# Kernel optimization log

Measured on AMD Instinct MI355X. Metric: run time of the kernel, lower is better.

The kernel has to match this reference:

```python
import jax, jax.numpy as jnp
import numpy as np

N, E, H, NOISE, T, G = 50000, 400000, 128, 64, 128, 16
EPS = 1e-5


def _graph_norm(x, seg, num_seg, w, b, ms):
    # PyG GraphNorm: per-graph mean/std with learnable mean_scale
    cnt = jnp.maximum(jax.ops.segment_sum(jnp.ones((x.shape[0],), x.dtype), seg, num_segments=num_seg), 1.0)
    mean = jax.ops.segment_sum(x, seg, num_segments=num_seg) / cnt[:, None]
    out = x - mean[seg] * ms
    var = jax.ops.segment_sum(out * out, seg, num_segments=num_seg) / cnt[:, None]
    return w * out / jnp.sqrt(var + EPS)[seg] + b


def _forward(features, noise_mapping_emb, time_emb,
             We, be, Wp, bp, Wq, bq, Wr, br, Wu, bu, Wv, bv,
             gnh_w, gnh_b, gnh_ms, gne_w, gne_b, gne_ms,
             Wt, bt, ln_w, ln_b, Wo, bo,
             edge_mapping_idx, batch):
    src, dst = edge_mapping_idx[0], edge_mapping_idx[1]
    nme = noise_mapping_emb @ We + be                                  # [E,H]
    e_hat = nme @ Wp + bp + (features @ Wq + bq)[src] + (features @ Wr + br)[dst]
    gates = jax.nn.sigmoid(e_hat)
    aggr = jax.ops.segment_sum((features @ Wv + bv)[dst] * gates, src, num_segments=N)
    h = _graph_norm(features @ Wu + bu + aggr, batch, G, gnh_w, gnh_b, gnh_ms)
    eseg = batch[src]                                                  # edge -> graph
    e = _graph_norm(e_hat, eseg, G, gne_w, gne_b, gne_ms)
    h = jax.nn.relu(h)
    e = jax.nn.relu(e)
    e = e + (jax.nn.relu(time_emb) @ Wt + bt)[eseg]
    h = features + h
    # out_layer: LayerNorm -> SiLU -> Linear
    mu = jnp.mean(e, axis=-1, keepdims=True)
    var = jnp.mean((e - mu) ** 2, axis=-1, keepdims=True)
    ln = (e - mu) / jnp.sqrt(var + EPS) * ln_w + ln_b
    e = nme + jax.nn.silu(ln) @ Wo + bo
    return h, e


def setup_inputs() -> dict:
    key = jax.random.key(0)
    ks = jax.random.split(key, 16)

    def lin(k, i, o):
        k1, k2 = jax.random.split(k)
        s = 1.0 / np.sqrt(i)
        return (jax.random.uniform(k1, (i, o), minval=-s, maxval=s, dtype=jnp.float32),
                jax.random.uniform(k2, (o,), minval=-s, maxval=s, dtype=jnp.float32))

    We, be = lin(ks[5], NOISE, H)
    Wp, bp = lin(ks[6], H, H)
    Wq, bq = lin(ks[7], H, H)
    Wr, br = lin(ks[8], H, H)
    Wu, bu = lin(ks[9], H, H)
    Wv, bv = lin(ks[10], H, H)
    Wt, bt = lin(ks[11], T, H)
    Wo, bo = lin(ks[12], H, H)
    ones = jnp.ones((H,), jnp.float32)
    zeros = jnp.zeros((H,), jnp.float32)
    return dict(
        features=jax.random.normal(ks[0], (N, H), dtype=jnp.float32),
        edge_mapping_idx=jax.random.randint(ks[1], (2, E), 0, N),
        noise_mapping_emb=jax.random.normal(ks[2], (E, NOISE), dtype=jnp.float32),
        time_emb=jax.random.normal(ks[3], (G, T), dtype=jnp.float32),
        batch=jnp.sort(jax.random.randint(ks[4], (N,), 0, G)),
        We=We, be=be, Wp=Wp, bp=bp, Wq=Wq, bq=bq, Wr=Wr, br=br,
        Wu=Wu, bu=bu, Wv=Wv, bv=bv,
        gnh_w=ones, gnh_b=zeros, gnh_ms=ones,
        gne_w=ones, gne_b=zeros, gne_ms=ones,
        Wt=Wt, bt=bt, ln_w=ones, ln_b=zeros, Wo=Wo, bo=bo,
    )


def reference(features, edge_mapping_idx, noise_mapping_emb, time_emb, batch,
              We, be, Wp, bp, Wq, bq, Wr, br, Wu, bu, Wv, bv,
              gnh_w, gnh_b, gnh_ms, gne_w, gne_b, gne_ms,
              Wt, bt, ln_w, ln_b, Wo, bo):
    return _forward(features, noise_mapping_emb, time_emb,
                    We, be, Wp, bp, Wq, bq, Wr, br, Wu, bu, Wv, bv,
                    gnh_w, gnh_b, gnh_ms, gne_w, gne_b, gne_ms,
                    Wt, bt, ln_w, ln_b, Wo, bo,
                    edge_mapping_idx, batch)
```

## Files before the change

kernel.cpp:

```cpp
#include <hip/hip_runtime.h>

#define NN 50000
#define NE 400000
#define HD 128
#define ND 64
#define GG 16
#define EPSV 1e-5f
#define ETILE 64
#define ETILE2 128

#define SLEN (2 * GG * HD + GG)
#define PSTRIDE 4352
#define EP 512
#define HP 256

typedef unsigned short u16;
typedef unsigned int   u32;
typedef unsigned char  u8;
typedef __attribute__((__ext_vector_type__(8))) __bf16 bf16x8;
typedef __attribute__((__ext_vector_type__(4))) float  f32x4;

__device__ __forceinline__ float us2f(u16 u) { return __uint_as_float(((u32)u) << 16); }
__device__ __forceinline__ u16 f2us(float f) {
    u32 u = __float_as_uint(f);
    u += 0x7fffu + ((u >> 16) & 1u);
    return (u16)(u >> 16);
}
__device__ __forceinline__ float sigmoidf_(float x) { return 1.f / (1.f + __expf(-x)); }

__global__ __launch_bounds__(256) void wep_kernel(
    const float* __restrict__ We, const float* __restrict__ Wp,
    const float* __restrict__ be, const float* __restrict__ bp,
    float* __restrict__ Wep, float* __restrict__ bep)
{
    __shared__ float wp[HD][HD];
    const int t = threadIdx.x;
    for (int i = t; i < HD * HD; i += 256) wp[i >> 7][i & 127] = Wp[i];
    __syncthreads();
    const int c = t & 127;
    for (int r = blockIdx.x * 4 + (t >> 7); r < (blockIdx.x + 1) * 4 && r < ND; r += 2) {
        float a = 0.f;
        for (int k = 0; k < HD; ++k) a = fmaf(We[r * HD + k], wp[k][c], a);
        Wep[r * HD + c] = a;
    }
    if (blockIdx.x == 0 && t < HD) {
        float a = bp[t];
        for (int k = 0; k < HD; ++k) a = fmaf(be[k], wp[k][t], a);
        bep[t] = a;
    }
}

__global__ __launch_bounds__(256) void prep_all_kernel(
    const float* __restrict__ Wq, const float* __restrict__ Wr,
    const float* __restrict__ Wv, const float* __restrict__ Wu,
    const float* __restrict__ Wo, const float* __restrict__ Wep,
    const float* __restrict__ We,
    u16* __restrict__ WqT, u16* __restrict__ WrT, u16* __restrict__ WvT,
    u16* __restrict__ WuT, u16* __restrict__ WoT, u16* __restrict__ WepT,
    u16* __restrict__ WeT)
{
    const float* in; u16* out; int K;
    switch (blockIdx.y) {
        case 0: in = Wq;  out = WqT;  K = HD; break;
        case 1: in = Wr;  out = WrT;  K = HD; break;
        case 2: in = Wv;  out = WvT;  K = HD; break;
        case 3: in = Wu;  out = WuT;  K = HD; break;
        case 4: in = Wo;  out = WoT;  K = HD; break;
        case 5: in = Wep; out = WepT; K = ND; break;
        default: in = We; out = WeT;  K = ND; break;
    }
    int idx = blockIdx.x * 256 + threadIdx.x;
    if (idx >= K * HD) return;
    int k = idx >> 7, n = idx & 127;
    out[n * K + k] = f2us(in[idx]);
}

__global__ __launch_bounds__(256) void hist_kernel(
    const int* __restrict__ srcArr, u32* __restrict__ deg)
{
    int e = blockIdx.x * 256 + threadIdx.x;
    if (e >= NE) return;
    atomicAdd(&deg[srcArr[e]], 1u);
}

#define SCAN_C 49
__global__ __launch_bounds__(1024) void scan_kernel(
    const u32* __restrict__ deg, int* __restrict__ start)
{
    __shared__ u32 sums[1024];
    const int t = threadIdx.x;
    const int i0 = t * SCAN_C;
    u32 tot = 0;
    for (int j = 0; j < SCAN_C; ++j) { int i = i0 + j; if (i < NN) tot += deg[i]; }
    sums[t] = tot;
    __syncthreads();
    for (int off = 1; off < 1024; off <<= 1) {
        u32 v = (t >= off) ? sums[t - off] : 0u;
        __syncthreads();
        sums[t] += v;
        __syncthreads();
    }
    u32 run = (t == 0) ? 0u : sums[t - 1];
    for (int j = 0; j < SCAN_C; ++j) {
        int i = i0 + j;
        if (i < NN) { start[i] = (int)run; run += deg[i]; }
    }
    if (t == 1023) start[NN] = (int)run;
}

__global__ __launch_bounds__(256) void scatter_kernel(
    const int* __restrict__ srcArr, const int* __restrict__ dstArr,
    const int* __restrict__ batch, const int* __restrict__ start,
    u32* __restrict__ cnt2, int* __restrict__ perm,
    int* __restrict__ src_csr, int* __restrict__ dst_csr,
    u8* __restrict__ g8csr)
{
    int e = blockIdx.x * 256 + threadIdx.x;
    if (e >= NE) return;
    int s = srcArr[e];
    u32 pos = atomicAdd(&cnt2[s], 1u);
    int j = start[s] + (int)pos;
    perm[j] = e;
    src_csr[j] = s;
    dst_csr[j] = dstArr[e];
    g8csr[j] = (u8)batch[s];
}

__global__ __launch_bounds__(256) void proj4_kernel(
    const float* __restrict__ feat,
    const u16* __restrict__ WqT, const u16* __restrict__ WrT,
    const u16* __restrict__ WvT, const u16* __restrict__ WuT,
    const float* __restrict__ bq, const float* __restrict__ br,
    const float* __restrict__ bv, const float* __restrict__ bu,
    u16* __restrict__ fq, u16* __restrict__ fr, u16* __restrict__ fv,
    float* __restrict__ fu32)
{
    __shared__ __align__(16) u16 As[ETILE * HD];
    const int t = threadIdx.x;
    const int rbase = blockIdx.x * ETILE;
    #pragma unroll
    for (int i = 0; i < 16; ++i) {
        int idx2 = t + i * 256;
        int row = idx2 >> 6, p = idx2 & 63;
        int grow = rbase + row;
        float2 v = make_float2(0.f, 0.f);
        if (grow < NN) v = *reinterpret_cast<const float2*>(&feat[(size_t)grow * HD + p * 2]);
        u32 pk = (u32)f2us(v.x) | ((u32)f2us(v.y) << 16);
        int off = (row * 256 + p * 4) ^ ((row & 7) << 4);
        *reinterpret_cast<u32*>(reinterpret_cast<char*>(As) + off) = pk;
    }
    __syncthreads();
    const int w = t >> 6, lane = t & 63;
    const int rt = w * 16, l15 = lane & 15, kg = lane >> 4;
    const int lrow = rt + l15;
    bf16x8 afr[4];
    #pragma unroll
    for (int kk = 0; kk < 4; ++kk) {
        int off = (lrow * 256 + (kk * 32 + kg * 8) * 2) ^ ((lrow & 7) << 4);
        afr[kk] = *reinterpret_cast<const bf16x8*>(reinterpret_cast<const char*>(As) + off);
    }
    const u16* WTs[4] = {WqT, WrT, WvT, WuT};
    const float* Bs2[4] = {bq, br, bv, bu};
    u16* Os[3] = {fq, fr, fv};
    #pragma unroll
    for (int m = 0; m < 4; ++m) {
        f32x4 acc[8];
        #pragma unroll
        for (int nt = 0; nt < 8; ++nt) { acc[nt][0]=0.f; acc[nt][1]=0.f; acc[nt][2]=0.f; acc[nt][3]=0.f; }
        const u16* W = WTs[m];
        #pragma unroll
        for (int nt = 0; nt < 8; ++nt) {
            #pragma unroll
            for (int kk = 0; kk < 4; ++kk) {
                bf16x8 b = *reinterpret_cast<const bf16x8*>(&W[(nt * 16 + l15) * HD + kk * 32 + kg * 8]);
                acc[nt] = __builtin_amdgcn_mfma_f32_16x16x32_bf16(afr[kk], b, acc[nt], 0, 0, 0);
            }
        }
        #pragma unroll
        for (int nt = 0; nt < 8; ++nt) {
            int gcol = nt * 16 + l15;
            float bias = Bs2[m][gcol];
            #pragma unroll
            for (int i = 0; i < 4; ++i) {
                int grow = rbase + rt + kg * 4 + i;
                if (grow < NN) {
                    float v = acc[nt][i] + bias;
                    if (m < 3) Os[m][(size_t)grow * HD + gcol] = f2us(v);
                    else       fu32[(size_t)grow * HD + gcol] = v;
                }
            }
        }
    }
}

__global__ __launch_bounds__(256) void ehat_kernel(
    const float* __restrict__ noise, const u16* __restrict__ WepT,
    const float* __restrict__ bep,
    const u16* __restrict__ fq, const u16* __restrict__ fr,
    const int* __restrict__ perm, const int* __restrict__ src_csr,
    const int* __restrict__ dst_csr,
    u16* __restrict__ ehat_csr)
{
    const int t = threadIdx.x;
    const int rbase = blockIdx.x * ETILE;
    const int w = t >> 6, lane = t & 63;
    const int rt = w * 16, l15 = lane & 15, kg = lane >> 4;
    const int jl = rbase + rt + l15;
    const int el = perm[jl];
    u32 an[2][4];
    #pragma unroll
    for (int kk = 0; kk < 2; ++kk) {
        const int c = kk * 32 + kg * 8;
        float4 n0 = *reinterpret_cast<const float4*>(&noise[(size_t)el * ND + c]);
        float4 n1 = *reinterpret_cast<const float4*>(&noise[(size_t)el * ND + c + 4]);
        an[kk][0] = (u32)f2us(n0.x) | ((u32)f2us(n0.y) << 16);
        an[kk][1] = (u32)f2us(n0.z) | ((u32)f2us(n0.w) << 16);
        an[kk][2] = (u32)f2us(n1.x) | ((u32)f2us(n1.y) << 16);
        an[kk][3] = (u32)f2us(n1.z) | ((u32)f2us(n1.w) << 16);
    }
    f32x4 acc[8];
    #pragma unroll
    for (int nt = 0; nt < 8; ++nt) {
        float b = bep[nt * 16 + l15];
        acc[nt][0] = b; acc[nt][1] = b; acc[nt][2] = b; acc[nt][3] = b;
    }
    #pragma unroll
    for (int nt = 0; nt < 8; ++nt) {
        #pragma unroll
        for (int kk = 0; kk < 2; ++kk) {
            bf16x8 b = *reinterpret_cast<const bf16x8*>(&WepT[(nt * 16 + l15) * ND + kk * 32 + kg * 8]);
            acc[nt] = __builtin_amdgcn_mfma_f32_16x16x32_bf16(
                *reinterpret_cast<const bf16x8*>(an[kk]), b, acc[nt], 0, 0, 0);
        }
    }
    #pragma unroll
    for (int i = 0; i < 4; ++i) {
        int jrow = rbase + rt + kg * 4 + i;
        int s = src_csr[jrow], d = dst_csr[jrow];
        #pragma unroll
        for (int nt = 0; nt < 8; ++nt) {
            int gcol = nt * 16 + l15;
            float v = acc[nt][i]
                    + us2f(fq[(size_t)s * HD + gcol]) + us2f(fr[(size_t)d * HD + gcol]);
            ehat_csr[(size_t)jrow * HD + gcol] = f2us(v);
        }
    }
}

__global__ __launch_bounds__(256) void aggr_kernel(
    const u16* __restrict__ ehat_csr, const u16* __restrict__ fv,
    const int* __restrict__ dst_csr, const int* __restrict__ start,
    float* __restrict__ xout)
{
    const int w = threadIdx.x >> 6, lane = threadIdx.x & 63;
    const int c0 = lane * 2;
    for (int node = blockIdx.x * 4 + w; node < NN; node += gridDim.x * 4) {
        int s0 = start[node], s1 = start[node + 1];
        float2 uv = *reinterpret_cast<const float2*>(&xout[(size_t)node * HD + c0]);
        float a0 = 0.f, a1 = 0.f;
        for (int j = s0; j < s1; ++j) {
            int d = dst_csr[j];
            u32 ev = *reinterpret_cast<const u32*>(&ehat_csr[(size_t)j * HD + c0]);
            u32 vv = *reinterpret_cast<const u32*>(&fv[(size_t)d * HD + c0]);
            a0 = fmaf(sigmoidf_(us2f((u16)ev)),         us2f((u16)vv),         a0);
            a1 = fmaf(sigmoidf_(us2f((u16)(ev >> 16))), us2f((u16)(vv >> 16)), a1);
        }
        *reinterpret_cast<float2*>(&xout[(size_t)node * HD + c0]) =
            make_float2(a0 + uv.x, a1 + uv.y);
    }
}

__global__ __launch_bounds__(256) void hstats_part_kernel(
    const float* __restrict__ xout, const int* __restrict__ batch,
    float* __restrict__ hpart)
{
    __shared__ float sm[SLEN];
    const int t = threadIdx.x;
    for (int i = t; i < SLEN; i += 256) sm[i] = 0.f;
    __syncthreads();
    const int cg = t & 15, rq = t >> 4;
    const int c8 = cg * 8;
    const int chunk = (NN + HP - 1) / HP;
    const int rstart = blockIdx.x * chunk;
    const int rend = min(NN, rstart + chunk);
    float s0[8], z0[8];
    #pragma unroll
    for (int p = 0; p < 8; ++p) { s0[p] = 0.f; z0[p] = 0.f; }
    float cn = 0.f;
    int curg = -1;
    for (int row = rstart + rq; row < rend; row += 16) {
        int g = batch[row];
        if (g != curg) {
            if (curg >= 0) {
                #pragma unroll
                for (int p = 0; p < 8; ++p) {
                    unsafeAtomicAdd(&sm[curg * HD + c8 + p], s0[p]);
                    unsafeAtomicAdd(&sm[2048 + curg * HD + c8 + p], z0[p]);
                    s0[p] = 0.f; z0[p] = 0.f;
                }
                if (cg == 0) { unsafeAtomicAdd(&sm[4096 + curg], cn); }
                cn = 0.f;
            }
            curg = g;
        }
        float4 xa = *reinterpret_cast<const float4*>(&xout[(size_t)row * HD + c8]);
        float4 xb = *reinterpret_cast<const float4*>(&xout[(size_t)row * HD + c8 + 4]);
        const float xs8[8] = {xa.x, xa.y, xa.z, xa.w, xb.x, xb.y, xb.z, xb.w};
        #pragma unroll
        for (int p = 0; p < 8; ++p) { s0[p] += xs8[p]; z0[p] = fmaf(xs8[p], xs8[p], z0[p]); }
        cn += (cg == 0) ? 1.f : 0.f;
    }
    if (curg >= 0) {
        #pragma unroll
        for (int p = 0; p < 8; ++p) {
            unsafeAtomicAdd(&sm[curg * HD + c8 + p], s0[p]);
            unsafeAtomicAdd(&sm[2048 + curg * HD + c8 + p], z0[p]);
        }
        if (cg == 0) { unsafeAtomicAdd(&sm[4096 + curg], cn); }
    }
    __syncthreads();
    float* dst = hpart + (size_t)blockIdx.x * PSTRIDE;
    for (int i = t; i < SLEN; i += 256) dst[i] = sm[i];
}

__global__ __launch_bounds__(512) void estats_part_kernel(
    const u16* __restrict__ ehat_csr, const u8* __restrict__ g8csr,
    float* __restrict__ epart)
{
    __shared__ float sm[SLEN];
    const int t = threadIdx.x;
    for (int i = t; i < SLEN; i += 512) sm[i] = 0.f;
    __syncthreads();
    const int cg = t & 15, rq = t >> 4;
    const int c8 = cg * 8;
    const int chunk = (NE + EP - 1) / EP;
    const int rstart = blockIdx.x * chunk;
    const int rend = min(NE, rstart + chunk);
    float s0[8], z0[8];
    #pragma unroll
    for (int p = 0; p < 8; ++p) { s0[p] = 0.f; z0[p] = 0.f; }
    float cn = 0.f;
    int curg = -1;
    for (int row = rstart + rq; row < rend; row += 32) {
        int g = (int)g8csr[row];
        if (g != curg) {
            if (curg >= 0) {
                #pragma unroll
                for (int p = 0; p < 8; ++p) {
                    unsafeAtomicAdd(&sm[curg * HD + c8 + p], s0[p]);
                    unsafeAtomicAdd(&sm[2048 + curg * HD + c8 + p], z0[p]);
                    s0[p] = 0.f; z0[p] = 0.f;
                }
                if (cg == 0) { unsafeAtomicAdd(&sm[4096 + curg], cn); }
                cn = 0.f;
            }
            curg = g;
        }
        uint4 ev = *reinterpret_cast<const uint4*>(&ehat_csr[(size_t)row * HD + c8]);
        const u32 wds[4] = {ev.x, ev.y, ev.z, ev.w};
        #pragma unroll
        for (int p2 = 0; p2 < 4; ++p2) {
            float x0 = us2f((u16)wds[p2]);
            float x1 = us2f((u16)(wds[p2] >> 16));
            s0[2 * p2]     += x0; z0[2 * p2]     = fmaf(x0, x0, z0[2 * p2]);
            s0[2 * p2 + 1] += x1; z0[2 * p2 + 1] = fmaf(x1, x1, z0[2 * p2 + 1]);
        }
        cn += (cg == 0) ? 1.f : 0.f;
    }
    if (curg >= 0) {
        #pragma unroll
        for (int p = 0; p < 8; ++p) {
            unsafeAtomicAdd(&sm[curg * HD + c8 + p], s0[p]);
            unsafeAtomicAdd(&sm[2048 + curg * HD + c8 + p], z0[p]);
        }
        if (cg == 0) { unsafeAtomicAdd(&sm[4096 + curg], cn); }
    }
    __syncthreads();
    float* dst = epart + (size_t)blockIdx.x * PSTRIDE;
    for (int i = t; i < SLEN; i += 512) dst[i] = sm[i];
}

__global__ __launch_bounds__(256) void reduce_part_kernel(
    const float* __restrict__ part, int P, int csz, float* __restrict__ out)
{
    int j = blockIdx.x * 256 + threadIdx.x;
    if (j >= SLEN) return;
    int p0 = blockIdx.y * csz;
    int p1 = min(P, p0 + csz);
    float a = 0.f;
    for (int p = p0; p < p1; ++p) a += part[(size_t)p * PSTRIDE + j];
    out[(size_t)blockIdx.y * PSTRIDE + j] = a;
}

__global__ __launch_bounds__(256) void finstats_kernel(
    const float* __restrict__ statsH, const float* __restrict__ statsE,
    const float* __restrict__ gnh_ms, const float* __restrict__ gne_ms,
    const float* __restrict__ gnh_w, const float* __restrict__ gnh_b,
    const float* __restrict__ gne_w, const float* __restrict__ gne_b,
    const float* __restrict__ ln_w, const float* __restrict__ ln_b,
    const float* __restrict__ be, const float* __restrict__ bo,
    float* __restrict__ SBh, float* __restrict__ SBe,
    float* __restrict__ LNWB, float* __restrict__ bsum)
{
    const int t = threadIdx.x;
    if (t < 64) {
        LNWB[4 * t]     = ln_w[2 * t];
        LNWB[4 * t + 1] = ln_b[2 * t];
        LNWB[4 * t + 2] = ln_w[2 * t + 1];
        LNWB[4 * t + 3] = ln_b[2 * t + 1];
    }
    if (t >= 64 && t < 192) bsum[t - 64] = be[t - 64] + bo[t - 64];
    for (int i = t; i < GG * HD; i += 256) {
        int g = i >> 7, c = i & 127;
        {
            float cnt = fmaxf(statsH[4096 + g], 1.f);
            float mean = statsH[i] / cnt;
            float ex2 = statsH[2048 + i] / cnt;
            float off = mean * gnh_ms[c];
            float var = ex2 - 2.f * off * mean + off * off;
            float S = gnh_w[c] * rsqrtf(var + EPSV);
            SBh[2 * i]     = S;
            SBh[2 * i + 1] = gnh_b[c] - off * S;
        }
        {
            float cnt = fmaxf(statsE[4096 + g], 1.f);
            float mean = statsE[i] / cnt;
            float ex2 = statsE[2048 + i] / cnt;
            float off = mean * gne_ms[c];
            float var = ex2 - 2.f * off * mean + off * off;
            float S = gne_w[c] * rsqrtf(var + EPSV);
            SBe[2 * i]     = S;
            SBe[2 * i + 1] = gne_b[c] - off * S;
        }
    }
}

__global__ __launch_bounds__(256) void tproj_kernel(
    const float* __restrict__ time_emb, const float* __restrict__ Wt,
    const float* __restrict__ bt, float* __restrict__ tproj)
{
    __shared__ float te[GG][HD];
    const int t = threadIdx.x;
    for (int i = t; i < GG * HD; i += 256) te[i >> 7][i & 127] = fmaxf(time_emb[i], 0.f);
    __syncthreads();
    const int c = t & 127, rb = t >> 7;
    float acc[8];
    #pragma unroll
    for (int j = 0; j < 8; ++j) acc[j] = 0.f;
    for (int k = 0; k < HD; ++k) {
        float wv = Wt[k * HD + c];
        #pragma unroll
        for (int j = 0; j < 8; ++j) acc[j] = fmaf(te[rb + 2 * j][k], wv, acc[j]);
    }
    float b = bt[c];
    #pragma unroll
    for (int j = 0; j < 8; ++j) tproj[(rb + 2 * j) * HD + c] = acc[j] + b;
}

__global__ __launch_bounds__(256) void hfinal_kernel(
    const float* __restrict__ feat, const int* __restrict__ batch,
    const float* __restrict__ SBh, float* hout_x)
{
    int i = blockIdx.x * 256 + threadIdx.x;
    size_t base = (size_t)i * 4;
    if (base >= (size_t)NN * HD) return;
    int row = (int)(base >> 7), c0 = (int)(base & 127);
    int g = batch[row];
    float4 fe = *reinterpret_cast<const float4*>(&feat[base]);
    float4 xv = *reinterpret_cast<const float4*>(&hout_x[base]);
    float4 sb0 = *reinterpret_cast<const float4*>(&SBh[(size_t)(g * HD + c0) * 2]);
    float4 sb1 = *reinterpret_cast<const float4*>(&SBh[(size_t)(g * HD + c0 + 2) * 2]);
    float4 ou;
    ou.x = fe.x + fmaxf(fmaf(xv.x, sb0.x, sb0.y), 0.f);
    ou.y = fe.y + fmaxf(fmaf(xv.y, sb0.z, sb0.w), 0.f);
    ou.z = fe.z + fmaxf(fmaf(xv.z, sb1.x, sb1.y), 0.f);
    ou.w = fe.w + fmaxf(fmaf(xv.w, sb1.z, sb1.w), 0.f);
    *reinterpret_cast<float4*>(&hout_x[base]) = ou;
}

__global__ __launch_bounds__(256) void efinal_kernel(
    const u16* __restrict__ ehat_csr, const u8* __restrict__ g8csr,
    const float* __restrict__ noise, const int* __restrict__ perm,
    const u16* __restrict__ WoT, const u16* __restrict__ WeT,
    const float* __restrict__ bsum,
    const float* __restrict__ SBe, const float* __restrict__ tproj,
    const float* __restrict__ LNWB,
    float* __restrict__ eout)
{
    const int t = threadIdx.x;
    const int rbase = blockIdx.x * ETILE2;
    const int w = t >> 6, lane = t & 63;
    const int l15 = lane & 15, kg = lane >> 4;
    const int rt = w * 32;

    u32 aw[2][4][4];
    u32 an[2][2][4];
    #pragma unroll
    for (int tile = 0; tile < 2; ++tile) {
        const int jl = rbase + rt + tile * 16 + l15;
        const int el = perm[jl];
        const int g = g8csr[jl];
        float v[4][8];
        float lsum = 0.f;
        #pragma unroll
        for (int kk = 0; kk < 4; ++kk) {
            const int c = kk * 32 + kg * 8;
            uint4 ev = *reinterpret_cast<const uint4*>(&ehat_csr[(size_t)jl * HD + c]);
            const u32 wds[4] = {ev.x, ev.y, ev.z, ev.w};
            #pragma unroll
            for (int p = 0; p < 4; ++p) {
                const int c2 = c + p * 2;
                float x0 = us2f((u16)wds[p]);
                float x1 = us2f((u16)(wds[p] >> 16));
                float4 sb = *reinterpret_cast<const float4*>(&SBe[(size_t)(g * HD + c2) * 2]);
                float2 tp = *reinterpret_cast<const float2*>(&tproj[g * HD + c2]);
                float a0 = fmaxf(fmaf(x0, sb.x, sb.y), 0.f) + tp.x;
                float a1 = fmaxf(fmaf(x1, sb.z, sb.w), 0.f) + tp.y;
                v[kk][p * 2]     = a0;
                v[kk][p * 2 + 1] = a1;
                lsum += a0 + a1;
            }
        }
        lsum += __shfl_xor(lsum, 16, 64);
        lsum += __shfl_xor(lsum, 32, 64);
        float mu = lsum * (1.f / 128.f);
        float sq = 0.f;
        #pragma unroll
        for (int kk = 0; kk < 4; ++kk)
            #pragma unroll
            for (int j = 0; j < 8; ++j) { float d = v[kk][j] - mu; sq = fmaf(d, d, sq); }
        sq += __shfl_xor(sq, 16, 64);
        sq += __shfl_xor(sq, 32, 64);
        float rstd = rsqrtf(sq * (1.f / 128.f) + EPSV);
        #pragma unroll
        for (int kk = 0; kk < 4; ++kk) {
            #pragma unroll
            for (int p = 0; p < 4; ++p) {
                float4 lnwb = *reinterpret_cast<const float4*>(&LNWB[(kk * 16 + kg * 4 + p) * 4]);
                float l0 = (v[kk][p * 2]     - mu) * rstd * lnwb.x + lnwb.y;
                float l1 = (v[kk][p * 2 + 1] - mu) * rstd * lnwb.z + lnwb.w;
                float s0 = l0 * sigmoidf_(l0);
                float s1 = l1 * sigmoidf_(l1);
                aw[tile][kk][p] = (u32)f2us(s0) | ((u32)f2us(s1) << 16);
            }
        }
        #pragma unroll
        for (int kk = 0; kk < 2; ++kk) {
            const int c = kk * 32 + kg * 8;
            float4 n0 = *reinterpret_cast<const float4*>(&noise[(size_t)el * ND + c]);
            float4 n1 = *reinterpret_cast<const float4*>(&noise[(size_t)el * ND + c + 4]);
            an[tile][kk][0] = (u32)f2us(n0.x) | ((u32)f2us(n0.y) << 16);
            an[tile][kk][1] = (u32)f2us(n0.z) | ((u32)f2us(n0.w) << 16);
            an[tile][kk][2] = (u32)f2us(n1.x) | ((u32)f2us(n1.y) << 16);
            an[tile][kk][3] = (u32)f2us(n1.z) | ((u32)f2us(n1.w) << 16);
        }
    }

    int prow[2][4];
    #pragma unroll
    for (int tile = 0; tile < 2; ++tile)
        #pragma unroll
        for (int i = 0; i < 4; ++i)
            prow[tile][i] = perm[rbase + rt + tile * 16 + kg * 4 + i];

    #pragma unroll
    for (int h = 0; h < 2; ++h) {
        f32x4 acc[2][4];
        #pragma unroll
        for (int q = 0; q < 4; ++q) {
            int gcol = (h * 4 + q) * 16 + l15;
            float bs = bsum[gcol];
            #pragma unroll
            for (int i = 0; i < 4; ++i) { acc[0][q][i] = bs; acc[1][q][i] = bs; }
        }
        #pragma unroll
        for (int q = 0; q < 4; ++q) {
            int nt = h * 4 + q;
            #pragma unroll
            for (int kk = 0; kk < 4; ++kk) {
                bf16x8 b = *reinterpret_cast<const bf16x8*>(&WoT[(nt * 16 + l15) * HD + kk * 32 + kg * 8]);
                acc[0][q] = __builtin_amdgcn_mfma_f32_16x16x32_bf16(
                    *reinterpret_cast<const bf16x8*>(aw[0][kk]), b, acc[0][q], 0, 0, 0);
                acc[1][q] = __builtin_amdgcn_mfma_f32_16x16x32_bf16(
                    *reinterpret_cast<const bf16x8*>(aw[1][kk]), b, acc[1][q], 0, 0, 0);
            }
            #pragma unroll
            for (int kk = 0; kk < 2; ++kk) {
                bf16x8 b = *reinterpret_cast<const bf16x8*>(&WeT[(nt * 16 + l15) * ND + kk * 32 + kg * 8]);
                acc[0][q] = __builtin_amdgcn_mfma_f32_16x16x32_bf16(
                    *reinterpret_cast<const bf16x8*>(an[0][kk]), b, acc[0][q], 0, 0, 0);
                acc[1][q] = __builtin_amdgcn_mfma_f32_16x16x32_bf16(
                    *reinterpret_cast<const bf16x8*>(an[1][kk]), b, acc[1][q], 0, 0, 0);
            }
        }
        #pragma unroll
        for (int tile = 0; tile < 2; ++tile) {
            #pragma unroll
            for (int q = 0; q < 4; ++q) {
                int gcol = (h * 4 + q) * 16 + l15;
                #pragma unroll
                for (int i = 0; i < 4; ++i) {
                    eout[(size_t)prow[tile][i] * HD + gcol] = acc[tile][q][i];
                }
            }
        }
    }
}

extern "C" void kernel_launch(void* const* d_in, const int* in_sizes, int n_in,
                              void* d_out, int out_size, void* d_ws, size_t ws_size,
                              hipStream_t stream)
{
    const float* feat     = (const float*)d_in[0];
    const int*   eidx     = (const int*)d_in[1];
    const float* noise    = (const float*)d_in[2];
    const float* time_emb = (const float*)d_in[3];
    const int*   batch    = (const int*)d_in[4];
    const float* We = (const float*)d_in[5],  *be = (const float*)d_in[6];
    const float* Wp = (const float*)d_in[7],  *bp = (const float*)d_in[8];
    const float* Wq = (const float*)d_in[9],  *bq = (const float*)d_in[10];
    const float* Wr = (const float*)d_in[11], *br = (const float*)d_in[12];
    const float* Wu = (const float*)d_in[13], *bu = (const float*)d_in[14];
    const float* Wv = (const float*)d_in[15], *bv = (const float*)d_in[16];
    const float* gnh_w = (const float*)d_in[17], *gnh_b = (const float*)d_in[18], *gnh_ms = (const float*)d_in[19];
    const float* gne_w = (const float*)d_in[20], *gne_b = (const float*)d_in[21], *gne_ms = (const float*)d_in[22];
    const float* Wt = (const float*)d_in[23], *bt = (const float*)d_in[24];
    const float* ln_w = (const float*)d_in[25], *ln_b = (const float*)d_in[26];
    const float* Wo = (const float*)d_in[27], *bo = (const float*)d_in[28];

    const int* srcArr = eidx;
    const int* dstArr = eidx + NE;

    float* hout = (float*)d_out;
    float* eout = hout + (size_t)NN * HD;

    char* ws = (char*)d_ws;
    size_t off = 0;
    auto take = [&](size_t bytes) -> char* {
        char* p = ws + off;
        off = (off + bytes + 255) & ~(size_t)255;
        return p;
    };
    u16* ehat = (u16*)take((size_t)NE * HD * 2);
    u16* fq = (u16*)take((size_t)NN * HD * 2);
    u16* fr = (u16*)take((size_t)NN * HD * 2);
    u16* fv = (u16*)take((size_t)NN * HD * 2);
    u8*  g8csr = (u8*)take((size_t)NE);
    u32* deg  = (u32*)take((size_t)2 * NN * 4);
    u32* cnt2 = deg + NN;
    int* start = (int*)take((size_t)(NN + 1) * 4);
    int* perm  = (int*)take((size_t)NE * 4);
    int* src_csr = (int*)take((size_t)NE * 4);
    int* dst_csr = (int*)take((size_t)NE * 4);
    float* Wep = (float*)take((size_t)ND * HD * 4);
    float* bep = (float*)take((size_t)HD * 4);
    u16* WqT = (u16*)take((size_t)HD * HD * 2);
    u16* WrT = (u16*)take((size_t)HD * HD * 2);
    u16* WvT = (u16*)take((size_t)HD * HD * 2);
    u16* WuT = (u16*)take((size_t)HD * HD * 2);
    u16* WoT = (u16*)take((size_t)HD * HD * 2);
    u16* WepT = (u16*)take((size_t)HD * ND * 2);
    u16* WeT  = (u16*)take((size_t)HD * ND * 2);
    float* statsH = (float*)take((size_t)PSTRIDE * 4);
    float* statsE = (float*)take((size_t)PSTRIDE * 4);
    float* tproj  = (float*)take((size_t)GG * HD * 4);
    float* SBh    = (float*)take((size_t)GG * HD * 8);
    float* SBe    = (float*)take((size_t)GG * HD * 8);
    float* LNWB   = (float*)take((size_t)64 * 4 * 4);
    float* bsum   = (float*)take((size_t)HD * 4);
    float* epart  = (float*)take((size_t)EP * PSTRIDE * 4);
    float* hpart  = (float*)take((size_t)HP * PSTRIDE * 4);
    float* etmp   = (float*)take((size_t)8 * PSTRIDE * 4);
    float* htmp   = (float*)take((size_t)8 * PSTRIDE * 4);

    hipMemsetAsync(deg, 0, (size_t)2 * NN * 4, stream);

    wep_kernel<<<16, 256, 0, stream>>>(We, Wp, be, bp, Wep, bep);
    prep_all_kernel<<<dim3(64, 7), 256, 0, stream>>>(Wq, Wr, Wv, Wu, Wo, Wep, We,
                                                     WqT, WrT, WvT, WuT, WoT, WepT, WeT);
    hist_kernel<<<(NE + 255) / 256, 256, 0, stream>>>(srcArr, deg);
    scan_kernel<<<1, 1024, 0, stream>>>(deg, start);
    scatter_kernel<<<(NE + 255) / 256, 256, 0, stream>>>(srcArr, dstArr, batch, start,
                                                         cnt2, perm, src_csr, dst_csr, g8csr);
    proj4_kernel<<<(NN + ETILE - 1) / ETILE, 256, 0, stream>>>(
        feat, WqT, WrT, WvT, WuT, bq, br, bv, bu, fq, fr, fv, hout);
    ehat_kernel<<<NE / ETILE, 256, 0, stream>>>(noise, WepT, bep, fq, fr,
                                                perm, src_csr, dst_csr, ehat);
    aggr_kernel<<<2048, 256, 0, stream>>>(ehat, fv, dst_csr, start, hout);
    hstats_part_kernel<<<HP, 256, 0, stream>>>(hout, batch, hpart);
    estats_part_kernel<<<EP, 512, 0, stream>>>(ehat, g8csr, epart);
    {
        dim3 gA((SLEN + 255) / 256, 8);
        reduce_part_kernel<<<gA, 256, 0, stream>>>(hpart, HP, HP / 8, htmp);
        reduce_part_kernel<<<gA, 256, 0, stream>>>(epart, EP, EP / 8, etmp);
        dim3 gB((SLEN + 255) / 256, 1);
        reduce_part_kernel<<<gB, 256, 0, stream>>>(htmp, 8, 8, statsH);
        reduce_part_kernel<<<gB, 256, 0, stream>>>(etmp, 8, 8, statsE);
    }
    tproj_kernel<<<1, 256, 0, stream>>>(time_emb, Wt, bt, tproj);
    finstats_kernel<<<1, 256, 0, stream>>>(statsH, statsE, gnh_ms, gne_ms,
                                           gnh_w, gnh_b, gne_w, gne_b,
                                           ln_w, ln_b, be, bo,
                                           SBh, SBe, LNWB, bsum);
    hfinal_kernel<<<(NN * HD / 4 + 255) / 256, 256, 0, stream>>>(feat, batch, SBh, hout);
    efinal_kernel<<<NE / ETILE2, 256, 0, stream>>>(ehat, g8csr, noise, perm, WoT, WeT,
                                                   bsum, SBe, tproj, LNWB, eout);
}
```

Measured before the change: 764.9 us.

## Split edge LayerNorm+SiLU prep from the output GEMM kernel

Moves the GraphNorm-apply, time-projection add, LayerNorm and SiLU for edges into a separate grid-stride kernel that overwrites the bf16 ehat buffer in place with SiLU activations. The output GEMM kernel then only loads ready bf16 A fragments and runs MFMAs, with the tile shrunk from 128 to 64 rows per block. The aim is to lower register pressure and raise occupancy in the MFMA kernel and to spread the elementwise work better across threads. In exchange it adds one more kernel launch and an extra read and write of the 400000x128 bf16 edge buffer.

Result: slower. 802.9 us (+5.0%).

```diff
diff --git a/kernel.cpp b/kernel.cpp
--- a/kernel.cpp
+++ b/kernel.cpp
@@ -7,7 +7,6 @@
 #define GG 16
 #define EPSV 1e-5f
 #define ETILE 64
-#define ETILE2 128
 
 #define SLEN (2 * GG * HD + GG)
 #define PSTRIDE 4352
@@ -478,131 +477,121 @@
     *reinterpret_cast<float4*>(&hout_x[base]) = ou;
 }
 
+__global__ __launch_bounds__(256) void eprep_kernel(
+    u16* __restrict__ ehat_csr, const u8* __restrict__ g8csr,
+    const float* __restrict__ SBe, const float* __restrict__ tproj,
+    const float* __restrict__ LNWB)
+{
+    const int t = threadIdx.x;
+    const int lane = t & 63;
+    const int cl = (lane & 15) * 8;
+    const int wrow = (t >> 6) * 4 + (lane >> 4);
+    for (int j = blockIdx.x * 16 + wrow; j < NE; j += gridDim.x * 16) {
+        int g = g8csr[j];
+        uint4 ev = *reinterpret_cast<const uint4*>(&ehat_csr[(size_t)j * HD + cl]);
+        const u32 wds[4] = {ev.x, ev.y, ev.z, ev.w};
+        float v[8];
+        float lsum = 0.f;
+        #pragma unroll
+        for (int p = 0; p < 4; ++p) {
+            int c2 = cl + p * 2;
+            float x0 = us2f((u16)wds[p]);
+            float x1 = us2f((u16)(wds[p] >> 16));
+            float4 sb = *reinterpret_cast<const float4*>(&SBe[(size_t)(g * HD + c2) * 2]);
+            float2 tp = *reinterpret_cast<const float2*>(&tproj[g * HD + c2]);
+            float a0 = fmaxf(fmaf(x0, sb.x, sb.y), 0.f) + tp.x;
+            float a1 = fmaxf(fmaf(x1, sb.z, sb.w), 0.f) + tp.y;
+            v[p * 2] = a0; v[p * 2 + 1] = a1;
+            lsum += a0 + a1;
+        }
+        lsum += __shfl_xor(lsum, 1, 64);
+        lsum += __shfl_xor(lsum, 2, 64);
+        lsum += __shfl_xor(lsum, 4, 64);
+        lsum += __shfl_xor(lsum, 8, 64);
+        float mu = lsum * (1.f / 128.f);
+        float sq = 0.f;
+        #pragma unroll
+        for (int p = 0; p < 8; ++p) { float d = v[p] - mu; sq = fmaf(d, d, sq); }
+        sq += __shfl_xor(sq, 1, 64);
+        sq += __shfl_xor(sq, 2, 64);
+        sq += __shfl_xor(sq, 4, 64);
+        sq += __shfl_xor(sq, 8, 64);
+        float rstd = rsqrtf(sq * (1.f / 128.f) + EPSV);
+        u32 ow[4];
+        #pragma unroll
+        for (int p = 0; p < 4; ++p) {
+            float4 lnwb = *reinterpret_cast<const float4*>(&LNWB[((cl >> 1) + p) * 4]);
+            float l0 = (v[p * 2]     - mu) * rstd * lnwb.x + lnwb.y;
+            float l1 = (v[p * 2 + 1] - mu) * rstd * lnwb.z + lnwb.w;
+            float s0 = l0 * sigmoidf_(l0);
+            float s1 = l1 * sigmoidf_(l1);
+            ow[p] = (u32)f2us(s0) | ((u32)f2us(s1) << 16);
+        }
+        *reinterpret_cast<uint4*>(&ehat_csr[(size_t)j * HD + cl]) =
+            make_uint4(ow[0], ow[1], ow[2], ow[3]);
+    }
+}
+
 __global__ __launch_bounds__(256) void efinal_kernel(
-    const u16* __restrict__ ehat_csr, const u8* __restrict__ g8csr,
-    const float* __restrict__ noise, const int* __restrict__ perm,
+    const u16* __restrict__ asilu, const float* __restrict__ noise,
+    const int* __restrict__ perm,
     const u16* __restrict__ WoT, const u16* __restrict__ WeT,
     const float* __restrict__ bsum,
-    const float* __restrict__ SBe, const float* __restrict__ tproj,
-    const float* __restrict__ LNWB,
     float* __restrict__ eout)
 {
     const int t = threadIdx.x;
-    const int rbase = blockIdx.x * ETILE2;
+    const int rbase = blockIdx.x * ETILE;
     const int w = t >> 6, lane = t & 63;
     const int l15 = lane & 15, kg = lane >> 4;
-    const int rt = w * 32;
-
-    u32 aw[2][4][4];
-    u32 an[2][2][4];
-    #pragma unroll
-    for (int tile = 0; tile < 2; ++tile) {
-        const int jl = rbase + rt + tile * 16 + l15;
-        const int el = perm[jl];
-        const int g = g8csr[jl];
-        float v[4][8];
-        float lsum = 0.f;
+    const int rt = w * 16;
+    const int jl = rbase + rt + l15;
+    const int el = perm[jl];
+
+    bf16x8 aw[4];
+    #pragma unroll
+    for (int kk = 0; kk < 4; ++kk)
+        aw[kk] = *reinterpret_cast<const bf16x8*>(&asilu[(size_t)jl * HD + kk * 32 + kg * 8]);
+    u32 an[2][4];
+    #pragma unroll
+    for (int kk = 0; kk < 2; ++kk) {
+        const int c = kk * 32 + kg * 8;
+        float4 n0 = *reinterpret_cast<const float4*>(&noise[(size_t)el * ND + c]);
+        float4 n1 = *reinterpret_cast<const float4*>(&noise[(size_t)el * ND + c + 4]);
+        an[kk][0] = (u32)f2us(n0.x) | ((u32)f2us(n0.y) << 16);
+        an[kk][1] = (u32)f2us(n0.z) | ((u32)f2us(n0.w) << 16);
+        an[kk][2] = (u32)f2us(n1.x) | ((u32)f2us(n1.y) << 16);
+        an[kk][3] = (u32)f2us(n1.z) | ((u32)f2us(n1.w) << 16);
+    }
+    int prow[4];
+    #pragma unroll
+    for (int i = 0; i < 4; ++i) prow[i] = perm[rbase + rt + kg * 4 + i];
+
+    f32x4 acc[8];
+    #pragma unroll
+    for (int nt = 0; nt < 8; ++nt) {
+        float bs = bsum[nt * 16 + l15];
+        acc[nt][0] = bs; acc[nt][1] = bs; acc[nt][2] = bs; acc[nt][3] = bs;
+    }
+    #pragma unroll
+    for (int nt = 0; nt < 8; ++nt) {
         #pragma unroll
         for (int kk = 0; kk < 4; ++kk) {
-            const int c = kk * 32 + kg * 8;
-            uint4 ev = *reinterpret_cast<const uint4*>(&ehat_csr[(size_t)jl * HD + c]);
-            const u32 wds[4] = {ev.x, ev.y, ev.z, ev.w};
-            #pragma unroll
-            for (int p = 0; p < 4; ++p) {
-                const int c2 = c + p * 2;
-                float x0 = us2f((u16)wds[p]);
-                float x1 = us2f((u16)(wds[p] >> 16));
-                float4 sb = *reinterpret_cast<const float4*>(&SBe[(size_t)(g * HD + c2) * 2]);
-                float2 tp = *reinterpret_cast<const float2*>(&tproj[g * HD + c2]);
-                float a0 = fmaxf(fmaf(x0, sb.x, sb.y), 0.f) + tp.x;
-                float a1 = fmaxf(fmaf(x1, sb.z, sb.w), 0.f) + tp.y;
-                v[kk][p * 2]     = a0;
-                v[kk][p * 2 + 1] = a1;
-                lsum += a0 + a1;
-            }
-        }
-        lsum += __shfl_xor(lsum, 16, 64);
-        lsum += __shfl_xor(lsum, 32, 64);
-        float mu = lsum * (1.f / 128.f);
-        float sq = 0.f;
-        #pragma unroll
-        for (int kk = 0; kk < 4; ++kk)
-            #pragma unroll
-            for (int j = 0; j < 8; ++j) { float d = v[kk][j] - mu; sq = fmaf(d, d, sq); }
-        sq += __shfl_xor(sq, 16, 64);
-        sq += __shfl_xor(sq, 32, 64);
-        float rstd = rsqrtf(sq * (1.f / 128.f) + EPSV);
-        #pragma unroll
-        for (int kk = 0; kk < 4; ++kk) {
-            #pragma unroll
-            for (int p = 0; p < 4; ++p) {
-                float4 lnwb = *reinterpret_cast<const float4*>(&LNWB[(kk * 16 + kg * 4 + p) * 4]);
-                float l0 = (v[kk][p * 2]     - mu) * rstd * lnwb.x + lnwb.y;
-                float l1 = (v[kk][p * 2 + 1] - mu) * rstd * lnwb.z + lnwb.w;
-                float s0 = l0 * sigmoidf_(l0);
-                float s1 = l1 * sigmoidf_(l1);
-                aw[tile][kk][p] = (u32)f2us(s0) | ((u32)f2us(s1) << 16);
-            }
+            bf16x8 b = *reinterpret_cast<const bf16x8*>(&WoT[(nt * 16 + l15) * HD + kk * 32 + kg * 8]);
+            acc[nt] = __builtin_amdgcn_mfma_f32_16x16x32_bf16(aw[kk], b, acc[nt], 0, 0, 0);
         }
         #pragma unroll
         for (int kk = 0; kk < 2; ++kk) {
-            const int c = kk * 32 + kg * 8;
-            float4 n0 = *reinterpret_cast<const float4*>(&noise[(size_t)el * ND + c]);
-            float4 n1 = *reinterpret_cast<const float4*>(&noise[(size_t)el * ND + c + 4]);
-            an[tile][kk][0] = (u32)f2us(n0.x) | ((u32)f2us(n0.y) << 16);
-            an[tile][kk][1] = (u32)f2us(n0.z) | ((u32)f2us(n0.w) << 16);
-            an[tile][kk][2] = (u32)f2us(n1.x) | ((u32)f2us(n1.y) << 16);
-            an[tile][kk][3] = (u32)f2us(n1.z) | ((u32)f2us(n1.w) << 16);
-        }
-    }
-
-    int prow[2][4];
-    #pragma unroll
-    for (int tile = 0; tile < 2; ++tile)
-        #pragma unroll
-        for (int i = 0; i < 4; ++i)
-            prow[tile][i] = perm[rbase + rt + tile * 16 + kg * 4 + i];
-
-    #pragma unroll
-    for (int h = 0; h < 2; ++h) {
-        f32x4 acc[2][4];
-        #pragma unroll
-        for (int q = 0; q < 4; ++q) {
-            int gcol = (h * 4 + q) * 16 + l15;
-            float bs = bsum[gcol];
-            #pragma unroll
-            for (int i = 0; i < 4; ++i) { acc[0][q][i] = bs; acc[1][q][i] = bs; }
-        }
-        #pragma unroll
-        for (int q = 0; q < 4; ++q) {
-            int nt = h * 4 + q;
-            #pragma unroll
-            for (int kk = 0; kk < 4; ++kk) {
-                bf16x8 b = *reinterpret_cast<const bf16x8*>(&WoT[(nt * 16 + l15) * HD + kk * 32 + kg * 8]);
-                acc[0][q] = __builtin_amdgcn_mfma_f32_16x16x32_bf16(
-                    *reinterpret_cast<const bf16x8*>(aw[0][kk]), b, acc[0][q], 0, 0, 0);
-                acc[1][q] = __builtin_amdgcn_mfma_f32_16x16x32_bf16(
-                    *reinterpret_cast<const bf16x8*>(aw[1][kk]), b, acc[1][q], 0, 0, 0);
-            }
-            #pragma unroll
-            for (int kk = 0; kk < 2; ++kk) {
-                bf16x8 b = *reinterpret_cast<const bf16x8*>(&WeT[(nt * 16 + l15) * ND + kk * 32 + kg * 8]);
-                acc[0][q] = __builtin_amdgcn_mfma_f32_16x16x32_bf16(
-                    *reinterpret_cast<const bf16x8*>(an[0][kk]), b, acc[0][q], 0, 0, 0);
-                acc[1][q] = __builtin_amdgcn_mfma_f32_16x16x32_bf16(
-                    *reinterpret_cast<const bf16x8*>(an[1][kk]), b, acc[1][q], 0, 0, 0);
-            }
-        }
-        #pragma unroll
-        for (int tile = 0; tile < 2; ++tile) {
-            #pragma unroll
-            for (int q = 0; q < 4; ++q) {
-                int gcol = (h * 4 + q) * 16 + l15;
-                #pragma unroll
-                for (int i = 0; i < 4; ++i) {
-                    eout[(size_t)prow[tile][i] * HD + gcol] = acc[tile][q][i];
-                }
-            }
+            bf16x8 b = *reinterpret_cast<const bf16x8*>(&WeT[(nt * 16 + l15) * ND + kk * 32 + kg * 8]);
+            acc[nt] = __builtin_amdgcn_mfma_f32_16x16x32_bf16(
+                *reinterpret_cast<const bf16x8*>(an[kk]), b, acc[nt], 0, 0, 0);
+        }
+    }
+    #pragma unroll
+    for (int nt = 0; nt < 8; ++nt) {
+        int gcol = nt * 16 + l15;
+        #pragma unroll
+        for (int i = 0; i < 4; ++i) {
+            eout[(size_t)prow[i] * HD + gcol] = acc[nt][i];
         }
     }
 }
@@ -702,7 +691,7 @@
                                            gnh_w, gnh_b, gne_w, gne_b,
                                            ln_w, ln_b, be, bo,
                                            SBh, SBe, LNWB, bsum);
+    eprep_kernel<<<2048, 256, 0, stream>>>(ehat, g8csr, SBe, tproj, LNWB);
     hfinal_kernel<<<(NN * HD / 4 + 255) / 256, 256, 0, stream>>>(feat, batch, SBh, hout);
-    efinal_kernel<<<NE / ETILE2, 256, 0, stream>>>(ehat, g8csr, noise, perm, WoT, WeT,
-                                                   bsum, SBe, tproj, LNWB, eout);
-}
+    efinal_kernel<<<NE / ETILE, 256, 0, stream>>>(ehat, noise, perm, WoT, WeT, bsum, eout);
+}
```
